# Performance work log

Hardware: AMD Instinct MI355X
Metric: run time of the kernel (lower is better)

## Reference

```python
import jax, jax.numpy as jnp
import numpy as np

EPSILON = 1e-5  # parameters.EPSILON
BN_EPS = 1e-5
N_NODES, N_EDGES, D = 50000, 400000, 128


def batch_norm(x, gamma, beta):
    # BatchNorm1d in training mode: biased batch statistics over dim 0
    m = jnp.mean(x, axis=0)
    v = jnp.var(x, axis=0)
    return (x - m) * jax.lax.rsqrt(v + BN_EPS) * gamma + beta


def setup_inputs() -> dict:
    key = jax.random.key(0)
    ks = jax.random.split(key, 16)
    s = 0.05
    d = D
    inp = {
        "h": jax.random.normal(ks[0], (N_NODES, d), jnp.float32),
        "e": jax.random.normal(ks[1], (N_EDGES, d), jnp.float32),
        "src": jax.random.randint(ks[2], (N_EDGES,), 0, N_NODES, jnp.int32),
        "dst": jax.random.randint(ks[3], (N_EDGES,), 0, N_NODES, jnp.int32),
        # weights stored [in, out]
        "W_emb_node": jax.random.normal(ks[4], (d, d)) * s,
        "W_emb_edge": jax.random.normal(ks[5], (d, d)) * s,
        "W_emb_eta": jax.random.normal(ks[6], (d, d)) * s,
        "Uw": jax.random.normal(ks[7], (d, d)) * s, "Ub": jnp.zeros((d,)),
        "Vw": jax.random.normal(ks[8], (d, d)) * s, "Vb": jnp.zeros((d,)),
        "W1w": jax.random.normal(ks[9], (d, d)) * s, "W1b": jnp.zeros((d,)),
        "W2w": jax.random.normal(ks[10], (d, d)) * s, "W2b": jnp.zeros((d,)),
        "W3w": jax.random.normal(ks[11], (d, d)) * s, "W3b": jnp.zeros((d,)),
        "h_gamma": jnp.ones((d,)), "h_beta": jnp.zeros((d,)),
        "e_gamma": jnp.ones((d,)), "e_beta": jnp.zeros((d,)),
    }
    return inp


def reference(h, e, src, dst, W_emb_node, W_emb_edge, W_emb_eta,
              Uw, Ub, Vw, Vb, W1w, W1b, W2w, W2b, W3w, W3b,
              h_gamma, h_beta, e_gamma, e_beta):
    n_nodes = h.shape[0]
    # node-level linear projections
    h_emb = h @ W_emb_node                 # [N, d]
    Uh = h @ Uw + Ub                       # [N, d]
    Vh = h @ Vw + Vb                       # [N, d]
    W2h = h @ W2w + W2b                    # [N, d]
    W3h = h @ W3w + W3b                    # [N, d]
    # edge-level
    e_emb = e @ W_emb_edge                 # [E, d]
    W1e = e @ W1w + W1b                    # [E, d]
    # edge update: e_ij = emb(e) + ReLU(BN(W1 e + W2 h_src + W3 h_dst))
    pre_e = W1e + W2h[src] + W3h[dst]      # gather [E, d]
    e_new = e_emb + jax.nn.relu(batch_norm(pre_e, e_gamma, e_beta))
    # gate: sigma_ij = embedding_eta(sigmoid(e_ij))
    sigma = jax.nn.sigmoid(e_new) @ W_emb_eta  # [E, d]
    # weighted-sum aggregation to destination nodes
    num = jax.ops.segment_sum(sigma * Vh[src], dst, num_segments=n_nodes)
    den = jax.ops.segment_sum(sigma, dst, num_segments=n_nodes)
    agg = num / (den + EPSILON)            # [N, d]
    h_new = h_emb + jax.nn.relu(batch_norm(Uh + agg, h_gamma, h_beta))
    return (h_new, e_new)
```

## Files before the change

### kernel.cpp

```cpp
#include <hip/hip_runtime.h>
#include <cstdint>
#include <cstddef>
#include <cmath>

#define DD 128

typedef short bf16x8 __attribute__((ext_vector_type(8)));
typedef float f32x4 __attribute__((ext_vector_type(4)));

static __device__ __forceinline__ short f2bf(float f){
  union { float f; uint32_t u; } v; v.f = f;
  uint32_t r = v.u + 0x7FFFu + ((v.u >> 16) & 1u);
  return (short)(r >> 16);
}
static __device__ __forceinline__ float bf2f(short h){
  union { uint32_t u; float f; } v; v.u = ((uint32_t)(uint16_t)h) << 16;
  return v.f;
}
static __device__ __forceinline__ double shfl_xor_f64(double v, int m){
  long long l = __double_as_longlong(v);
  int lo = (int)(l & 0xffffffffLL);
  int hi = (int)((unsigned long long)l >> 32);
  lo = __shfl_xor(lo, m, 64);
  hi = __shfl_xor(hi, m, 64);
  return __longlong_as_double(((long long)hi << 32) | (unsigned long long)(unsigned int)lo);
}

template<int EP>
__global__ __launch_bounds__(256, 2) void dgemm_k(
    const float* __restrict__ X,
    const float* __restrict__ W1, const float* __restrict__ b1,
    const float* __restrict__ W2, const float* __restrict__ b2,
    float* __restrict__ Y1, float* __restrict__ Y2,
    int M, int nTiles,
    const int* __restrict__ src, const int* __restrict__ dst,
    const float* __restrict__ T2, const float* __restrict__ T3,
    double* __restrict__ eSum, double* __restrict__ eSumSq)
{
  __shared__ float sA[128][36];
  __shared__ float sW1[32][128];
  __shared__ float sW2[32][128];
  __shared__ double redS[(EP == 1) ? 4 : 1][32][4];
  __shared__ double redQ[(EP == 1) ? 4 : 1][32][4];

  const int tid = threadIdx.x, tx = tid & 31, ty = tid >> 5;
  const int c0 = tx * 4, r0 = ty * 16;
  const int lane = tid & 63, wv = tid >> 6;

  float b1c[4], b2c[4];
  #pragma unroll
  for (int j = 0; j < 4; ++j){
    b1c[j] = b1 ? b1[c0 + j] : 0.0f;
    b2c[j] = b2 ? b2[c0 + j] : 0.0f;
  }
  double st_s[4] = {0,0,0,0}, st_q[4] = {0,0,0,0};

  #pragma unroll 1
  for (int tile = blockIdx.x; tile < nTiles; tile += gridDim.x){
    const int rowBase = tile * 128;
    float acc1[16][4], acc2[16][4];
    #pragma unroll
    for (int r = 0; r < 16; ++r)
      #pragma unroll
      for (int j = 0; j < 4; ++j){ acc1[r][j] = 0.0f; acc2[r][j] = 0.0f; }

    #pragma unroll 1
    for (int h = 0; h < 4; ++h){
      #pragma unroll
      for (int m = 0; m < 4; ++m){
        int k = ty + 8 * m;
        *(f32x4*)&sW1[k][c0] = *(const f32x4*)&W1[(size_t)(h*32 + k) * DD + c0];
        *(f32x4*)&sW2[k][c0] = *(const f32x4*)&W2[(size_t)(h*32 + k) * DD + c0];
      }
      {
        int r = tid >> 1, koff = (tid & 1) * 16;
        int ar = rowBase + r; if (ar >= M) ar = M - 1;
        const float* xp = X + (size_t)ar * DD + h*32 + koff;
        #pragma unroll
        for (int q = 0; q < 4; ++q)
          *(f32x4*)&sA[r][koff + q*4] = *(const f32x4*)(xp + q*4);
      }
      __syncthreads();

      #pragma unroll
      for (int q = 0; q < 8; ++q){
        f32x4 wA0 = *(const f32x4*)&sW1[4*q + 0][c0];
        f32x4 wA1 = *(const f32x4*)&sW1[4*q + 1][c0];
        f32x4 wA2 = *(const f32x4*)&sW1[4*q + 2][c0];
        f32x4 wA3 = *(const f32x4*)&sW1[4*q + 3][c0];
        f32x4 wB0 = *(const f32x4*)&sW2[4*q + 0][c0];
        f32x4 wB1 = *(const f32x4*)&sW2[4*q + 1][c0];
        f32x4 wB2 = *(const f32x4*)&sW2[4*q + 2][c0];
        f32x4 wB3 = *(const f32x4*)&sW2[4*q + 3][c0];
        #pragma unroll
        for (int r = 0; r < 16; ++r){
          f32x4 a = *(const f32x4*)&sA[r0 + r][4*q];
          #pragma unroll
          for (int j = 0; j < 4; ++j){
            float t1 = acc1[r][j];
            t1 = fmaf(a[0], wA0[j], t1); t1 = fmaf(a[1], wA1[j], t1);
            t1 = fmaf(a[2], wA2[j], t1); t1 = fmaf(a[3], wA3[j], t1);
            acc1[r][j] = t1;
            float t2 = acc2[r][j];
            t2 = fmaf(a[0], wB0[j], t2); t2 = fmaf(a[1], wB1[j], t2);
            t2 = fmaf(a[2], wB2[j], t2); t2 = fmaf(a[3], wB3[j], t2);
            acc2[r][j] = t2;
          }
        }
      }
      __syncthreads();
    }

    #pragma unroll
    for (int r = 0; r < 16; ++r){
      int row = rowBase + r0 + r;
      if (row < M){
        size_t base = (size_t)row * DD + c0;
        if (EP == 0){
          f32x4 o1, o2;
          #pragma unroll
          for (int j = 0; j < 4; ++j){ o1[j] = acc1[r][j] + b1c[j]; o2[j] = acc2[r][j] + b2c[j]; }
          *(f32x4*)&Y1[base] = o1;
          *(f32x4*)&Y2[base] = o2;
        } else {
          int s = src[row], d = dst[row];
          f32x4 t2v = *(const f32x4*)&T2[(size_t)s * DD + c0];
          f32x4 t3v = *(const f32x4*)&T3[(size_t)d * DD + c0];
          f32x4 o1, o2;
          #pragma unroll
          for (int j = 0; j < 4; ++j){
            o1[j] = ((acc1[r][j] + b1c[j]) + t2v[j]) + t3v[j];
            st_s[j] += (double)o1[j];
            st_q[j] += (double)o1[j] * (double)o1[j];
            o2[j] = acc2[r][j];
          }
          *(f32x4*)&Y1[base] = o1;
          *(f32x4*)&Y2[base] = o2;
        }
      }
    }
  }

  if (EP == 1){
    #pragma unroll
    for (int j = 0; j < 4; ++j){
      st_s[j] += shfl_xor_f64(st_s[j], 32);
      st_q[j] += shfl_xor_f64(st_q[j], 32);
    }
    if (lane < 32){
      #pragma unroll
      for (int j = 0; j < 4; ++j){ redS[wv][lane][j] = st_s[j]; redQ[wv][lane][j] = st_q[j]; }
    }
    __syncthreads();
    if (tid < 128){
      int txx = tid >> 2, j = tid & 3;
      double s = 0.0, q = 0.0;
      #pragma unroll
      for (int w = 0; w < 4; ++w){ s += redS[w][txx][j]; q += redQ[w][txx][j]; }
      atomicAdd(&eSum[txx*4 + j], s);
      atomicAdd(&eSumSq[txx*4 + j], q);
    }
  }
}

__global__ __launch_bounds__(256, 2) void sgemm_k(
    const float* __restrict__ preE, const float* __restrict__ eEmb,
    const float* __restrict__ Weta,
    float* __restrict__ eNew, float* __restrict__ sigmaOut,
    const float* __restrict__ mF, const float* __restrict__ rF,
    const float* __restrict__ gF, const float* __restrict__ bF,
    int M, int nTiles)
{
  __shared__ float sA[128][68];
  __shared__ float sW[64][128];
  const int tid = threadIdx.x, tx = tid & 31, ty = tid >> 5;
  const int c0 = tx * 4, r0 = ty * 16;

  #pragma unroll 1
  for (int tile = blockIdx.x; tile < nTiles; tile += gridDim.x){
    const int rowBase = tile * 128;
    float acc[16][4];
    #pragma unroll
    for (int r = 0; r < 16; ++r)
      #pragma unroll
      for (int j = 0; j < 4; ++j) acc[r][j] = 0.0f;

    #pragma unroll 1
    for (int h = 0; h < 2; ++h){
      {
        int kk = ty * 8;
        #pragma unroll
        for (int q = 0; q < 8; ++q)
          *(f32x4*)&sW[kk + q][c0] = *(const f32x4*)&Weta[(size_t)(h*64 + kk + q) * DD + c0];
      }
      {
        int r = tid >> 1, koff = (tid & 1) * 32;
        int ar = rowBase + r;
        int gcb = h*64 + koff;
        const float* pp = preE + (size_t)ar * DD + gcb;
        const float* ep = eEmb + (size_t)ar * DD + gcb;
        float* np = eNew + (size_t)ar * DD + gcb;
        #pragma unroll
        for (int q = 0; q < 8; ++q){
          f32x4 pe = *(const f32x4*)(pp + q*4);
          f32x4 em = *(const f32x4*)(ep + q*4);
          f32x4 mm = *(const f32x4*)&mF[gcb + q*4];
          f32x4 rr = *(const f32x4*)&rF[gcb + q*4];
          f32x4 gg = *(const f32x4*)&gF[gcb + q*4];
          f32x4 bb = *(const f32x4*)&bF[gcb + q*4];
          f32x4 en, sg;
          #pragma unroll
          for (int j = 0; j < 4; ++j){
            float xm  = pe[j] - mm[j];
            float t1  = xm * rr[j];
            float t2v = t1 * gg[j];
            float t3v = t2v + bb[j];
            float t = fmaxf(t3v, 0.0f);
            en[j] = em[j] + t;
            sg[j] = 1.0f / (1.0f + expf(-en[j]));
          }
          *(f32x4*)(np + q*4) = en;
          *(f32x4*)&sA[r][koff + q*4] = sg;
        }
      }
      __syncthreads();

      #pragma unroll 2
      for (int q = 0; q < 16; ++q){
        f32x4 b0 = *(const f32x4*)&sW[4*q + 0][c0];
        f32x4 b1 = *(const f32x4*)&sW[4*q + 1][c0];
        f32x4 b2 = *(const f32x4*)&sW[4*q + 2][c0];
        f32x4 b3 = *(const f32x4*)&sW[4*q + 3][c0];
        #pragma unroll
        for (int r = 0; r < 16; ++r){
          f32x4 a = *(const f32x4*)&sA[r0 + r][4*q];
          #pragma unroll
          for (int j = 0; j < 4; ++j){
            float t = acc[r][j];
            t = fmaf(a[0], b0[j], t); t = fmaf(a[1], b1[j], t);
            t = fmaf(a[2], b2[j], t); t = fmaf(a[3], b3[j], t);
            acc[r][j] = t;
          }
        }
      }
      __syncthreads();
    }

    #pragma unroll
    for (int r = 0; r < 16; ++r){
      int row = rowBase + r0 + r;
      f32x4 o;
      #pragma unroll
      for (int j = 0; j < 4; ++j) o[j] = acc[r][j];
      *(f32x4*)&sigmaOut[(size_t)row * DD + c0] = o;
    }
  }
}

__global__ void hist_k(const int* __restrict__ dst, int NE, int* __restrict__ counts){
  int i = blockIdx.x * blockDim.x + threadIdx.x;
  if (i < NE) atomicAdd(&counts[dst[i]], 1);
}

__global__ __launch_bounds__(1024, 1) void scan_k(const int* __restrict__ counts, int NN,
                                                  int* __restrict__ rowStart, int* __restrict__ cursor){
  __shared__ int part[1024];
  const int T = 1024, t = threadIdx.x;
  const int chunk = (NN + T - 1) / T;
  const int lo = t * chunk;
  const int hi = (lo + chunk < NN) ? lo + chunk : NN;
  int s = 0;
  for (int i = lo; i < hi; ++i) s += counts[i];
  part[t] = s;
  __syncthreads();
  for (int off = 1; off < T; off <<= 1){
    int v = (t >= off) ? part[t - off] : 0;
    __syncthreads();
    part[t] += v;
    __syncthreads();
  }
  int run = (t == 0) ? 0 : part[t - 1];
  for (int i = lo; i < hi; ++i){ rowStart[i] = run; cursor[i] = run; run += counts[i]; }
  if (t == T - 1) rowStart[NN] = run;
}

__global__ void place_k(const int* __restrict__ dst, int NE,
                        int* __restrict__ cursor, int* __restrict__ edgeIdx){
  int i = blockIdx.x * blockDim.x + threadIdx.x;
  if (i < NE){ int p = atomicAdd(&cursor[dst[i]], 1); edgeIdx[p] = i; }
}

__global__ __launch_bounds__(256, 4) void gather_k(
    const float* __restrict__ sigma, const float* __restrict__ Vh,
    const int* __restrict__ rowStart, const int* __restrict__ edgeIdx,
    const int* __restrict__ srcArr,
    const float* __restrict__ Uh, float* __restrict__ preH, int NN)
{
  const int lane = threadIdx.x & 63, wv = threadIdx.x >> 6;
  for (int node = blockIdx.x * 4 + wv; node < NN; node += gridDim.x * 4){
    const int beg = rowStart[node], end = rowStart[node + 1];
    float den0 = 0.f, den1 = 0.f, num0 = 0.f, num1 = 0.f;
    for (int eb = beg; eb < end; eb += 4){
      const int nE = end - eb;
      float sg0[4], sg1[4], vh0[4], vh1[4];
      #pragma unroll
      for (int q = 0; q < 4; ++q){
        if (q < nE){
          int eid = edgeIdx[eb + q];
          int s = srcArr[eid];
          sg0[q] = sigma[(size_t)eid * DD + lane];
          sg1[q] = sigma[(size_t)eid * DD + 64 + lane];
          vh0[q] = Vh[(size_t)s * DD + lane];
          vh1[q] = Vh[(size_t)s * DD + 64 + lane];
        } else { sg0[q] = 0.f; sg1[q] = 0.f; vh0[q] = 0.f; vh1[q] = 0.f; }
      }
      #pragma unroll
      for (int q = 0; q < 4; ++q){
        den0 += sg0[q]; den1 += sg1[q];
        num0 = fmaf(sg0[q], vh0[q], num0);
        num1 = fmaf(sg1[q], vh1[q], num1);
      }
    }
    const size_t b = (size_t)node * DD;
    preH[b + lane]      = Uh[b + lane]      + num0 / (den0 + 1e-5f);
    preH[b + 64 + lane] = Uh[b + 64 + lane] + num1 / (den1 + 1e-5f);
  }
}

__global__ void finalizeE_k(const double* __restrict__ sum, const double* __restrict__ sumsq,
                            double M, float* __restrict__ mF, float* __restrict__ rF)
{
  int c = threadIdx.x;
  double m = sum[c] / M;
  double v = sumsq[c] / M - m * m;
  float vf = (float)v;
  mF[c] = (float)m;
  rF[c] = 1.0f / sqrtf(vf + 1e-5f);
}

__global__ void stats64_k(const float* __restrict__ X, int M,
                          double* __restrict__ sum, double* __restrict__ sumsq)
{
  const int col = threadIdx.x & 127;
  const int half = threadIdx.x >> 7;
  double s = 0.0, q = 0.0;
  for (int r = blockIdx.x * 2 + half; r < M; r += gridDim.x * 2){
    double v = (double)X[(size_t)r * DD + col];
    s += v; q += v * v;
  }
  __shared__ double sS[256], sQ[256];
  sS[threadIdx.x] = s; sQ[threadIdx.x] = q;
  __syncthreads();
  if (half == 0){
    atomicAdd(&sum[col],   sS[col] + sS[col + 128]);
    atomicAdd(&sumsq[col], sQ[col] + sQ[col + 128]);
  }
}

__global__ void finalize64_k(const double* __restrict__ sum, const double* __restrict__ sumsq,
                             double M, const float* __restrict__ gamma, const float* __restrict__ beta,
                             double* __restrict__ scale, double* __restrict__ shift)
{
  int c = threadIdx.x;
  double m = sum[c] / M;
  double var = sumsq[c] / M - m * m;
  double sc = (double)gamma[c] / sqrt(var + 1e-5);
  scale[c] = sc;
  shift[c] = (double)beta[c] - m * sc;
}

__global__ __launch_bounds__(256, 2) void hfinal_mfma_k(
    const float* __restrict__ X, const float* __restrict__ W,
    float* __restrict__ Y, int M, int rowTiles,
    const float* __restrict__ preH,
    const double* __restrict__ hSc, const double* __restrict__ hSh)
{
  const int tid = threadIdx.x;
  const int lane = tid & 63;
  const int wv = tid >> 6;
  const int l15 = lane & 15;
  const int lg = lane >> 4;
  const int colBase = blockIdx.y * 64;

  __shared__ short sW[2][64][136];
  for (int t = tid; t < 64 * 128; t += 256){
    int k = t >> 6, nl = t & 63;
    float w = W[k * DD + colBase + nl];
    short hi = f2bf(w);
    sW[0][nl][k] = hi;
    sW[1][nl][k] = f2bf(w - bf2f(hi));
  }
  __syncthreads();

  bf16x8 Bhi[4][4], Blo[4][4];
  #pragma unroll
  for (int ct = 0; ct < 4; ++ct)
    #pragma unroll
    for (int ks = 0; ks < 4; ++ks){
      Bhi[ct][ks] = *(const bf16x8*)&sW[0][ct*16 + l15][ks*32 + lg*8];
      Blo[ct][ks] = *(const bf16x8*)&sW[1][ct*16 + l15][ks*32 + lg*8];
    }

  for (int rt = blockIdx.x; rt < rowTiles; rt += gridDim.x){
    int arow = rt * 64 + wv * 16 + l15;
    if (arow >= M) arow = M - 1;
    const f32x4* xr = (const f32x4*)(X + (size_t)arow * DD);

    bf16x8 Ahi[4], Alo[4];
    #pragma unroll
    for (int ks = 0; ks < 4; ++ks){
      f32x4 a0 = xr[ks*8 + lg*2];
      f32x4 a1 = xr[ks*8 + lg*2 + 1];
      float av[8];
      #pragma unroll
      for (int j = 0; j < 4; ++j){ av[j] = a0[j]; av[4+j] = a1[j]; }
      #pragma unroll
      for (int j = 0; j < 8; ++j){
        short hi = f2bf(av[j]);
        Ahi[ks][j] = hi;
        Alo[ks][j] = f2bf(av[j] - bf2f(hi));
      }
    }

    f32x4 acc[4];
    #pragma unroll
    for (int ct = 0; ct < 4; ++ct) acc[ct] = (f32x4){0.f, 0.f, 0.f, 0.f};
    #pragma unroll
    for (int ct = 0; ct < 4; ++ct)
      #pragma unroll
      for (int ks = 0; ks < 4; ++ks){
        acc[ct] = __builtin_amdgcn_mfma_f32_16x16x32_bf16(Ahi[ks], Bhi[ct][ks], acc[ct], 0, 0, 0);
        acc[ct] = __builtin_amdgcn_mfma_f32_16x16x32_bf16(Ahi[ks], Blo[ct][ks], acc[ct], 0, 0, 0);
        acc[ct] = __builtin_amdgcn_mfma_f32_16x16x32_bf16(Alo[ks], Bhi[ct][ks], acc[ct], 0, 0, 0);
      }

    const int r0 = rt * 64 + wv * 16 + lg * 4;
    #pragma unroll
    for (int reg = 0; reg < 4; ++reg){
      int r = r0 + reg;
      if (r < M){
        #pragma unroll
        for (int ct = 0; ct < 4; ++ct){
          int c = colBase + ct*16 + l15;
          double t = (double)preH[(size_t)r * DD + c] * hSc[c] + hSh[c];
          float tv = t > 0.0 ? (float)t : 0.0f;
          Y[(size_t)r * DD + c] = acc[ct][reg] + tv;
        }
      }
    }
  }
}

extern "C" void kernel_launch(void* const* d_in, const int* in_sizes, int n_in,
                              void* d_out, int out_size, void* d_ws, size_t ws_size,
                              hipStream_t stream)
{
  const float* h  = (const float*)d_in[0];
  const float* e  = (const float*)d_in[1];
  const int* src  = (const int*)d_in[2];
  const int* dst  = (const int*)d_in[3];
  const float* Wemb_n   = (const float*)d_in[4];
  const float* Wemb_e   = (const float*)d_in[5];
  const float* Wemb_eta = (const float*)d_in[6];
  const float* Uw  = (const float*)d_in[7];  const float* Ub  = (const float*)d_in[8];
  const float* Vw  = (const float*)d_in[9];  const float* Vb  = (const float*)d_in[10];
  const float* W1w = (const float*)d_in[11]; const float* W1b = (const float*)d_in[12];
  const float* W2w = (const float*)d_in[13]; const float* W2b = (const float*)d_in[14];
  const float* W3w = (const float*)d_in[15]; const float* W3b = (const float*)d_in[16];
  const float* h_gamma = (const float*)d_in[17]; const float* h_beta = (const float*)d_in[18];
  const float* e_gamma = (const float*)d_in[19]; const float* e_beta = (const float*)d_in[20];

  const int NN = in_sizes[0] / DD;
  const int NE = in_sizes[2];

  char* wsp = (char*)d_ws;
  float* W2h    = (float*)wsp;  wsp += (size_t)NN * DD * sizeof(float);
  float* W3h    = (float*)wsp;  wsp += (size_t)NN * DD * sizeof(float);
  float* Vh     = (float*)wsp;  wsp += (size_t)NN * DD * sizeof(float);
  float* embSig = (float*)wsp;  wsp += (size_t)NE * DD * sizeof(float);
  double* stats = (double*)wsp; wsp += 6 * DD * sizeof(double);
  double* eSum = stats;        double* eSumSq = stats + DD;
  double* hSum = stats + 2*DD; double* hSumSq = stats + 3*DD;
  double* hScale = stats + 4*DD; double* hShift = stats + 5*DD;
  float* mF = (float*)wsp;   wsp += DD * sizeof(float);
  float* rF = (float*)wsp;   wsp += DD * sizeof(float);
  int* counts   = (int*)wsp; wsp += (size_t)NN * sizeof(int);
  int* rowStart = (int*)wsp; wsp += ((size_t)NN + 1) * sizeof(int);
  int* cursor   = (int*)wsp; wsp += (size_t)NN * sizeof(int);
  int* edgeIdx  = (int*)wsp; wsp += (size_t)NE * sizeof(int);

  float* h_new_out = (float*)d_out;
  float* e_out     = (float*)d_out + (size_t)NN * DD;

  const int tN = (NN + 127) / 128;
  const int tE = (NE + 127) / 128;
  const int rtN64 = (NN + 63) / 64;
  dim3 blk(256);

  hipMemsetAsync(stats, 0, (size_t)4 * DD * sizeof(double), stream);
  hipMemsetAsync(counts, 0, (size_t)NN * sizeof(int), stream);

  hist_k<<<(NE + 255) / 256, blk, 0, stream>>>(dst, NE, counts);
  scan_k<<<1, 1024, 0, stream>>>(counts, NN, rowStart, cursor);
  place_k<<<(NE + 255) / 256, blk, 0, stream>>>(dst, NE, cursor, edgeIdx);

  dgemm_k<0><<<tN, blk, 0, stream>>>(h, Uw, Ub, Vw, Vb, h_new_out, Vh, NN, tN,
      nullptr, nullptr, nullptr, nullptr, nullptr, nullptr);
  dgemm_k<0><<<tN, blk, 0, stream>>>(h, W2w, W2b, W3w, W3b, W2h, W3h, NN, tN,
      nullptr, nullptr, nullptr, nullptr, nullptr, nullptr);

  dgemm_k<1><<<1024, blk, 0, stream>>>(e, W1w, W1b, Wemb_e, nullptr, e_out, embSig,
      NE, tE, src, dst, W2h, W3h, eSum, eSumSq);

  finalizeE_k<<<1, 128, 0, stream>>>(eSum, eSumSq, (double)NE, mF, rF);

  sgemm_k<<<tE, blk, 0, stream>>>(e_out, embSig, Wemb_eta, e_out, embSig,
      mF, rF, e_gamma, e_beta, NE, tE);

  gather_k<<<(NN + 3) / 4, blk, 0, stream>>>(embSig, Vh, rowStart, edgeIdx, src,
      h_new_out, h_new_out, NN);

  stats64_k<<<512, blk, 0, stream>>>(h_new_out, NN, hSum, hSumSq);
  finalize64_k<<<1, 128, 0, stream>>>(hSum, hSumSq, (double)NN, h_gamma, h_beta, hScale, hShift);

  hfinal_mfma_k<<<dim3(rtN64, 2), blk, 0, stream>>>(h, Wemb_n, h_new_out, NN, rtN64,
      h_new_out, hScale, hShift);
}
```

Baseline: 1.251 ms.

## Use 512-thread blocks with halved per-thread tiles, merge node GEMM launches

Thread blocks for the FP32 GEMM kernels go from 256 to 512 threads, and each thread now holds 8 rows instead of 16. This halves accumulator registers and lets more waves fit per CU to hide latency. The two node-level dgemm launches are merged into one grid, using blockIdx.y to pick the weight set, and sgemm now uses a persistent grid of 1024 blocks with smaller K chunks. The gather loop is widened to 8 edges per iteration for more memory-level parallelism. Costs are more shared-memory loads per FMA, since the register tile is smaller, and more barriers.

```diff
diff --git a/kernel.cpp b/kernel.cpp
--- a/kernel.cpp
+++ b/kernel.cpp
@@ -27,11 +27,14 @@
 }
 
 template<int EP>
-__global__ __launch_bounds__(256, 2) void dgemm_k(
+__global__ __launch_bounds__(512, 4) void dgemm_k(
     const float* __restrict__ X,
-    const float* __restrict__ W1, const float* __restrict__ b1,
-    const float* __restrict__ W2, const float* __restrict__ b2,
-    float* __restrict__ Y1, float* __restrict__ Y2,
+    const float* __restrict__ W1a, const float* __restrict__ b1a,
+    const float* __restrict__ W2a, const float* __restrict__ b2a,
+    float* __restrict__ Y1a, float* __restrict__ Y2a,
+    const float* __restrict__ W1B, const float* __restrict__ b1B,
+    const float* __restrict__ W2B, const float* __restrict__ b2B,
+    float* __restrict__ Y1B, float* __restrict__ Y2B,
     int M, int nTiles,
     const int* __restrict__ src, const int* __restrict__ dst,
     const float* __restrict__ T2, const float* __restrict__ T3,
@@ -40,12 +43,18 @@
   __shared__ float sA[128][36];
   __shared__ float sW1[32][128];
   __shared__ float sW2[32][128];
-  __shared__ double redS[(EP == 1) ? 4 : 1][32][4];
-  __shared__ double redQ[(EP == 1) ? 4 : 1][32][4];
+  __shared__ double redS[(EP == 1) ? 8 : 1][32][4];
+  __shared__ double redQ[(EP == 1) ? 8 : 1][32][4];
 
   const int tid = threadIdx.x, tx = tid & 31, ty = tid >> 5;
-  const int c0 = tx * 4, r0 = ty * 16;
+  const int c0 = tx * 4, r0 = ty * 8;
   const int lane = tid & 63, wv = tid >> 6;
+
+  const float *W1 = W1a, *b1 = b1a, *W2 = W2a, *b2 = b2a;
+  float *Y1 = Y1a, *Y2 = Y2a;
+  if (EP == 0 && blockIdx.y == 1){
+    W1 = W1B; b1 = b1B; W2 = W2B; b2 = b2B; Y1 = Y1B; Y2 = Y2B;
+  }
 
   float b1c[4], b2c[4];
   #pragma unroll
@@ -58,27 +67,27 @@
   #pragma unroll 1
   for (int tile = blockIdx.x; tile < nTiles; tile += gridDim.x){
     const int rowBase = tile * 128;
-    float acc1[16][4], acc2[16][4];
-    #pragma unroll
-    for (int r = 0; r < 16; ++r)
+    float acc1[8][4], acc2[8][4];
+    #pragma unroll
+    for (int r = 0; r < 8; ++r)
       #pragma unroll
       for (int j = 0; j < 4; ++j){ acc1[r][j] = 0.0f; acc2[r][j] = 0.0f; }
 
     #pragma unroll 1
     for (int h = 0; h < 4; ++h){
       #pragma unroll
-      for (int m = 0; m < 4; ++m){
-        int k = ty + 8 * m;
-        *(f32x4*)&sW1[k][c0] = *(const f32x4*)&W1[(size_t)(h*32 + k) * DD + c0];
-        *(f32x4*)&sW2[k][c0] = *(const f32x4*)&W2[(size_t)(h*32 + k) * DD + c0];
+      for (int m = 0; m < 2; ++m){
+        int idx = tid + m * 512;
+        int k = idx >> 5, cc = (idx & 31) * 4;
+        *(f32x4*)&sW1[k][cc] = *(const f32x4*)&W1[(size_t)(h*32 + k) * DD + cc];
+        *(f32x4*)&sW2[k][cc] = *(const f32x4*)&W2[(size_t)(h*32 + k) * DD + cc];
       }
       {
-        int r = tid >> 1, koff = (tid & 1) * 16;
+        int r = tid >> 2, koff = (tid & 3) * 8;
         int ar = rowBase + r; if (ar >= M) ar = M - 1;
         const float* xp = X + (size_t)ar * DD + h*32 + koff;
-        #pragma unroll
-        for (int q = 0; q < 4; ++q)
-          *(f32x4*)&sA[r][koff + q*4] = *(const f32x4*)(xp + q*4);
+        *(f32x4*)&sA[r][koff]     = *(const f32x4*)(xp);
+        *(f32x4*)&sA[r][koff + 4] = *(const f32x4*)(xp + 4);
       }
       __syncthreads();
 
@@ -93,7 +102,7 @@
         f32x4 wB2 = *(const f32x4*)&sW2[4*q + 2][c0];
         f32x4 wB3 = *(const f32x4*)&sW2[4*q + 3][c0];
         #pragma unroll
-        for (int r = 0; r < 16; ++r){
+        for (int r = 0; r < 8; ++r){
           f32x4 a = *(const f32x4*)&sA[r0 + r][4*q];
           #pragma unroll
           for (int j = 0; j < 4; ++j){
@@ -112,7 +121,7 @@
     }
 
     #pragma unroll
-    for (int r = 0; r < 16; ++r){
+    for (int r = 0; r < 8; ++r){
       int row = rowBase + r0 + r;
       if (row < M){
         size_t base = (size_t)row * DD + c0;
@@ -156,14 +165,14 @@
       int txx = tid >> 2, j = tid & 3;
       double s = 0.0, q = 0.0;
       #pragma unroll
-      for (int w = 0; w < 4; ++w){ s += redS[w][txx][j]; q += redQ[w][txx][j]; }
+      for (int w = 0; w < 8; ++w){ s += redS[w][txx][j]; q += redQ[w][txx][j]; }
       atomicAdd(&eSum[txx*4 + j], s);
       atomicAdd(&eSumSq[txx*4 + j], q);
     }
   }
 }
 
-__global__ __launch_bounds__(256, 2) void sgemm_k(
+__global__ __launch_bounds__(512, 4) void sgemm_k(
     const float* __restrict__ preE, const float* __restrict__ eEmb,
     const float* __restrict__ Weta,
     float* __restrict__ eNew, float* __restrict__ sigmaOut,
@@ -171,37 +180,37 @@
     const float* __restrict__ gF, const float* __restrict__ bF,
     int M, int nTiles)
 {
-  __shared__ float sA[128][68];
-  __shared__ float sW[64][128];
+  __shared__ float sA[128][36];
+  __shared__ float sW[32][128];
   const int tid = threadIdx.x, tx = tid & 31, ty = tid >> 5;
-  const int c0 = tx * 4, r0 = ty * 16;
+  const int c0 = tx * 4, r0 = ty * 8;
 
   #pragma unroll 1
   for (int tile = blockIdx.x; tile < nTiles; tile += gridDim.x){
     const int rowBase = tile * 128;
-    float acc[16][4];
-    #pragma unroll
-    for (int r = 0; r < 16; ++r)
+    float acc[8][4];
+    #pragma unroll
+    for (int r = 0; r < 8; ++r)
       #pragma unroll
       for (int j = 0; j < 4; ++j) acc[r][j] = 0.0f;
 
     #pragma unroll 1
-    for (int h = 0; h < 2; ++h){
+    for (int h = 0; h < 4; ++h){
+      #pragma unroll
+      for (int m = 0; m < 2; ++m){
+        int idx = tid + m * 512;
+        int k = idx >> 5, cc = (idx & 31) * 4;
+        *(f32x4*)&sW[k][cc] = *(const f32x4*)&Weta[(size_t)(h*32 + k) * DD + cc];
+      }
       {
-        int kk = ty * 8;
-        #pragma unroll
-        for (int q = 0; q < 8; ++q)
-          *(f32x4*)&sW[kk + q][c0] = *(const f32x4*)&Weta[(size_t)(h*64 + kk + q) * DD + c0];
-      }
-      {
-        int r = tid >> 1, koff = (tid & 1) * 32;
+        int r = tid >> 2, koff = (tid & 3) * 8;
         int ar = rowBase + r;
-        int gcb = h*64 + koff;
+        int gcb = h*32 + koff;
         const float* pp = preE + (size_t)ar * DD + gcb;
         const float* ep = eEmb + (size_t)ar * DD + gcb;
         float* np = eNew + (size_t)ar * DD + gcb;
         #pragma unroll
-        for (int q = 0; q < 8; ++q){
+        for (int q = 0; q < 2; ++q){
           f32x4 pe = *(const f32x4*)(pp + q*4);
           f32x4 em = *(const f32x4*)(ep + q*4);
           f32x4 mm = *(const f32x4*)&mF[gcb + q*4];
@@ -225,14 +234,14 @@
       }
       __syncthreads();
 
-      #pragma unroll 2
-      for (int q = 0; q < 16; ++q){
+      #pragma unroll
+      for (int q = 0; q < 8; ++q){
         f32x4 b0 = *(const f32x4*)&sW[4*q + 0][c0];
         f32x4 b1 = *(const f32x4*)&sW[4*q + 1][c0];
         f32x4 b2 = *(const f32x4*)&sW[4*q + 2][c0];
         f32x4 b3 = *(const f32x4*)&sW[4*q + 3][c0];
         #pragma unroll
-        for (int r = 0; r < 16; ++r){
+        for (int r = 0; r < 8; ++r){
           f32x4 a = *(const f32x4*)&sA[r0 + r][4*q];
           #pragma unroll
           for (int j = 0; j < 4; ++j){
@@ -247,7 +256,7 @@
     }
 
     #pragma unroll
-    for (int r = 0; r < 16; ++r){
+    for (int r = 0; r < 8; ++r){
       int row = rowBase + r0 + r;
       f32x4 o;
       #pragma unroll
@@ -300,11 +309,11 @@
   for (int node = blockIdx.x * 4 + wv; node < NN; node += gridDim.x * 4){
     const int beg = rowStart[node], end = rowStart[node + 1];
     float den0 = 0.f, den1 = 0.f, num0 = 0.f, num1 = 0.f;
-    for (int eb = beg; eb < end; eb += 4){
+    for (int eb = beg; eb < end; eb += 8){
       const int nE = end - eb;
-      float sg0[4], sg1[4], vh0[4], vh1[4];
-      #pragma unroll
-      for (int q = 0; q < 4; ++q){
+      float sg0[8], sg1[8], vh0[8], vh1[8];
+      #pragma unroll
+      for (int q = 0; q < 8; ++q){
         if (q < nE){
           int eid = edgeIdx[eb + q];
           int s = srcArr[eid];
@@ -315,7 +324,7 @@
         } else { sg0[q] = 0.f; sg1[q] = 0.f; vh0[q] = 0.f; vh1[q] = 0.f; }
       }
       #pragma unroll
-      for (int q = 0; q < 4; ++q){
+      for (int q = 0; q < 8; ++q){
         den0 += sg0[q]; den1 += sg1[q];
         num0 = fmaf(sg0[q], vh0[q], num0);
         num1 = fmaf(sg1[q], vh1[q], num1);
@@ -495,34 +504,36 @@
   const int tN = (NN + 127) / 128;
   const int tE = (NE + 127) / 128;
   const int rtN64 = (NN + 63) / 64;
-  dim3 blk(256);
+  dim3 blk256(256), blk512(512);
 
   hipMemsetAsync(stats, 0, (size_t)4 * DD * sizeof(double), stream);
   hipMemsetAsync(counts, 0, (size_t)NN * sizeof(int), stream);
 
-  hist_k<<<(NE + 255) / 256, blk, 0, stream>>>(dst, NE, counts);
+  hist_k<<<(NE + 255) / 256, blk256, 0, stream>>>(dst, NE, counts);
   scan_k<<<1, 1024, 0, stream>>>(counts, NN, rowStart, cursor);
-  place_k<<<(NE + 255) / 256, blk, 0, stream>>>(dst, NE, cursor, edgeIdx);
-
-  dgemm_k<0><<<tN, blk, 0, stream>>>(h, Uw, Ub, Vw, Vb, h_new_out, Vh, NN, tN,
-      nullptr, nullptr, nullptr, nullptr, nullptr, nullptr);
-  dgemm_k<0><<<tN, blk, 0, stream>>>(h, W2w, W2b, W3w, W3b, W2h, W3h, NN, tN,
-      nullptr, nullptr, nullptr, nullptr, nullptr, nullptr);
-
-  dgemm_k<1><<<1024, blk, 0, stream>>>(e, W1w, W1b, Wemb_e, nullptr, e_out, embSig,
+  place_k<<<(NE + 255) / 256, blk256, 0, stream>>>(dst, NE, cursor, edgeIdx);
+
+  dgemm_k<0><<<dim3(256, 2), blk512, 0, stream>>>(h,
+      Uw, Ub, Vw, Vb, h_new_out, Vh,
+      W2w, W2b, W3w, W3b, W2h, W3h,
+      NN, tN, nullptr, nullptr, nullptr, nullptr, nullptr, nullptr);
+
+  dgemm_k<1><<<1024, blk512, 0, stream>>>(e,
+      W1w, W1b, Wemb_e, nullptr, e_out, embSig,
+      nullptr, nullptr, nullptr, nullptr, nullptr, nullptr,
       NE, tE, src, dst, W2h, W3h, eSum, eSumSq);
 
   finalizeE_k<<<1, 128, 0, stream>>>(eSum, eSumSq, (double)NE, mF, rF);
 
-  sgemm_k<<<tE, blk, 0, stream>>>(e_out, embSig, Wemb_eta, e_out, embSig,
+  sgemm_k<<<1024, blk512, 0, stream>>>(e_out, embSig, Wemb_eta, e_out, embSig,
       mF, rF, e_gamma, e_beta, NE, tE);
 
-  gather_k<<<(NN + 3) / 4, blk, 0, stream>>>(embSig, Vh, rowStart, edgeIdx, src,
+  gather_k<<<(NN + 3) / 4, blk256, 0, stream>>>(embSig, Vh, rowStart, edgeIdx, src,
       h_new_out, h_new_out, NN);
 
-  stats64_k<<<512, blk, 0, stream>>>(h_new_out, NN, hSum, hSumSq);
+  stats64_k<<<512, blk256, 0, stream>>>(h_new_out, NN, hSum, hSumSq);
   finalize64_k<<<1, 128, 0, stream>>>(hSum, hSumSq, (double)NN, h_gamma, h_beta, hScale, hShift);
 
-  hfinal_mfma_k<<<dim3(rtN64, 2), blk, 0, stream>>>(h, Wemb_n, h_new_out, NN, rtN64,
+  hfinal_mfma_k<<<dim3(rtN64, 2), blk256, 0, stream>>>(h, Wemb_n, h_new_out, NN, rtN64,
       h_new_out, hScale, hShift);
 }
```

Result: slower. 1.370 ms (+9.6%).

## Split dual-output GEMMs into single-output GEMMs and shrink sigmoid-GEMM tiles

Applied to the files above, without the earlier changes.

Replaces the dual-weight GEMM kernel with a single-weight version, so each node projection and the edge embedding run as separate launches with half the accumulators and shared memory. The sigmoid/eta GEMM now uses 32-wide K chunks, caches BN parameters in shared memory, and runs on a persistent 1024-block grid. The gather loop processes 8 edges per iteration instead of 4. Register pressure and LDS use go down, which can raise occupancy, but X (h and e) is read twice as often, and the edge tensor e is now read twice.

```diff
diff --git a/kernel.cpp b/kernel.cpp
--- a/kernel.cpp
+++ b/kernel.cpp
@@ -27,84 +27,72 @@
 }
 
 template<int EP>
-__global__ __launch_bounds__(256, 2) void dgemm_k(
-    const float* __restrict__ X,
-    const float* __restrict__ W1, const float* __restrict__ b1,
-    const float* __restrict__ W2, const float* __restrict__ b2,
-    float* __restrict__ Y1, float* __restrict__ Y2,
+__global__ __launch_bounds__(256, 2) void fgemm_k(
+    const float* __restrict__ X, const float* __restrict__ W,
+    const float* __restrict__ bias, float* __restrict__ Y,
     int M, int nTiles,
     const int* __restrict__ src, const int* __restrict__ dst,
     const float* __restrict__ T2, const float* __restrict__ T3,
     double* __restrict__ eSum, double* __restrict__ eSumSq)
 {
   __shared__ float sA[128][36];
-  __shared__ float sW1[32][128];
-  __shared__ float sW2[32][128];
+  __shared__ float sW[32][128];
   __shared__ double redS[(EP == 1) ? 4 : 1][32][4];
   __shared__ double redQ[(EP == 1) ? 4 : 1][32][4];
 
   const int tid = threadIdx.x, tx = tid & 31, ty = tid >> 5;
   const int c0 = tx * 4, r0 = ty * 16;
   const int lane = tid & 63, wv = tid >> 6;
-
-  float b1c[4], b2c[4];
+  const int sa_r = tid >> 1, sa_k = (tid & 1) * 16;
+  const int sw_k = tid >> 3, sw_c = (tid & 7) * 16;
+
+  float bias_c[4];
   #pragma unroll
-  for (int j = 0; j < 4; ++j){
-    b1c[j] = b1 ? b1[c0 + j] : 0.0f;
-    b2c[j] = b2 ? b2[c0 + j] : 0.0f;
-  }
+  for (int j = 0; j < 4; ++j) bias_c[j] = bias ? bias[c0 + j] : 0.0f;
+
   double st_s[4] = {0,0,0,0}, st_q[4] = {0,0,0,0};
 
   #pragma unroll 1
   for (int tile = blockIdx.x; tile < nTiles; tile += gridDim.x){
     const int rowBase = tile * 128;
-    float acc1[16][4], acc2[16][4];
+    float acc[16][4];
     #pragma unroll
     for (int r = 0; r < 16; ++r)
       #pragma unroll
-      for (int j = 0; j < 4; ++j){ acc1[r][j] = 0.0f; acc2[r][j] = 0.0f; }
+      for (int j = 0; j < 4; ++j) acc[r][j] = 0.0f;
 
     #pragma unroll 1
     for (int h = 0; h < 4; ++h){
-      #pragma unroll
-      for (int m = 0; m < 4; ++m){
-        int k = ty + 8 * m;
-        *(f32x4*)&sW1[k][c0] = *(const f32x4*)&W1[(size_t)(h*32 + k) * DD + c0];
-        *(f32x4*)&sW2[k][c0] = *(const f32x4*)&W2[(size_t)(h*32 + k) * DD + c0];
-      }
       {
-        int r = tid >> 1, koff = (tid & 1) * 16;
-        int ar = rowBase + r; if (ar >= M) ar = M - 1;
-        const float* xp = X + (size_t)ar * DD + h*32 + koff;
-        #pragma unroll
-        for (int q = 0; q < 4; ++q)
-          *(f32x4*)&sA[r][koff + q*4] = *(const f32x4*)(xp + q*4);
+        const float* wp = W + (size_t)(h*32 + sw_k) * DD + sw_c;
+        #pragma unroll
+        for (int i = 0; i < 4; ++i)
+          *(f32x4*)&sW[sw_k][sw_c + i*4] = *(const f32x4*)(wp + i*4);
+      }
+      {
+        int ar = rowBase + sa_r; if (ar >= M) ar = M - 1;
+        const float* xp = X + (size_t)ar * DD + h*32 + sa_k;
+        #pragma unroll
+        for (int i = 0; i < 4; ++i)
+          *(f32x4*)&sA[sa_r][sa_k + i*4] = *(const f32x4*)(xp + i*4);
       }
       __syncthreads();
 
       #pragma unroll
       for (int q = 0; q < 8; ++q){
-        f32x4 wA0 = *(const f32x4*)&sW1[4*q + 0][c0];
-        f32x4 wA1 = *(const f32x4*)&sW1[4*q + 1][c0];
-        f32x4 wA2 = *(const f32x4*)&sW1[4*q + 2][c0];
-        f32x4 wA3 = *(const f32x4*)&sW1[4*q + 3][c0];
-        f32x4 wB0 = *(const f32x4*)&sW2[4*q + 0][c0];
-        f32x4 wB1 = *(const f32x4*)&sW2[4*q + 1][c0];
-        f32x4 wB2 = *(const f32x4*)&sW2[4*q + 2][c0];
-        f32x4 wB3 = *(const f32x4*)&sW2[4*q + 3][c0];
+        f32x4 b0 = *(const f32x4*)&sW[4*q + 0][c0];
+        f32x4 b1 = *(const f32x4*)&sW[4*q + 1][c0];
+        f32x4 b2 = *(const f32x4*)&sW[4*q + 2][c0];
+        f32x4 b3 = *(const f32x4*)&sW[4*q + 3][c0];
         #pragma unroll
         for (int r = 0; r < 16; ++r){
           f32x4 a = *(const f32x4*)&sA[r0 + r][4*q];
           #pragma unroll
           for (int j = 0; j < 4; ++j){
-            float t1 = acc1[r][j];
-            t1 = fmaf(a[0], wA0[j], t1); t1 = fmaf(a[1], wA1[j], t1);
-            t1 = fmaf(a[2], wA2[j], t1); t1 = fmaf(a[3], wA3[j], t1);
-            acc1[r][j] = t1;
-            float t2 = acc2[r][j];
-            t2 = fmaf(a[0], wB0[j], t2); t2 = fmaf(a[1], wB1[j], t2);
-            t2 = fmaf(a[2], wB2[j], t2); t2 = fmaf(a[3], wB3[j], t2);
-            acc2[r][j] = t2;
+            float t = acc[r][j];
+            t = fmaf(a[0], b0[j], t); t = fmaf(a[1], b1[j], t);
+            t = fmaf(a[2], b2[j], t); t = fmaf(a[3], b3[j], t);
+            acc[r][j] = t;
           }
         }
       }
@@ -117,25 +105,22 @@
       if (row < M){
         size_t base = (size_t)row * DD + c0;
         if (EP == 0){
-          f32x4 o1, o2;
+          f32x4 o;
           #pragma unroll
-          for (int j = 0; j < 4; ++j){ o1[j] = acc1[r][j] + b1c[j]; o2[j] = acc2[r][j] + b2c[j]; }
-          *(f32x4*)&Y1[base] = o1;
-          *(f32x4*)&Y2[base] = o2;
+          for (int j = 0; j < 4; ++j) o[j] = acc[r][j] + bias_c[j];
+          *(f32x4*)&Y[base] = o;
         } else {
           int s = src[row], d = dst[row];
-          f32x4 t2v = *(const f32x4*)&T2[(size_t)s * DD + c0];
-          f32x4 t3v = *(const f32x4*)&T3[(size_t)d * DD + c0];
-          f32x4 o1, o2;
+          f32x4 t2 = *(const f32x4*)&T2[(size_t)s * DD + c0];
+          f32x4 t3 = *(const f32x4*)&T3[(size_t)d * DD + c0];
+          f32x4 o;
           #pragma unroll
           for (int j = 0; j < 4; ++j){
-            o1[j] = ((acc1[r][j] + b1c[j]) + t2v[j]) + t3v[j];
-            st_s[j] += (double)o1[j];
-            st_q[j] += (double)o1[j] * (double)o1[j];
-            o2[j] = acc2[r][j];
+            o[j] = ((acc[r][j] + bias_c[j]) + t2[j]) + t3[j];
+            st_s[j] += (double)o[j];
+            st_q[j] += (double)o[j] * (double)o[j];
           }
-          *(f32x4*)&Y1[base] = o1;
-          *(f32x4*)&Y2[base] = o2;
+          *(f32x4*)&Y[base] = o;
         }
       }
     }
@@ -163,7 +148,7 @@
   }
 }
 
-__global__ __launch_bounds__(256, 2) void sgemm_k(
+__global__ __launch_bounds__(256, 2) void psgemm_k(
     const float* __restrict__ preE, const float* __restrict__ eEmb,
     const float* __restrict__ Weta,
     float* __restrict__ eNew, float* __restrict__ sigmaOut,
@@ -171,14 +156,26 @@
     const float* __restrict__ gF, const float* __restrict__ bF,
     int M, int nTiles)
 {
-  __shared__ float sA[128][68];
-  __shared__ float sW[64][128];
+  __shared__ float sA[128][36];
+  __shared__ float sW[32][128];
+  __shared__ float sBN[4][128];
+
   const int tid = threadIdx.x, tx = tid & 31, ty = tid >> 5;
   const int c0 = tx * 4, r0 = ty * 16;
+  const int sa_r = tid >> 1, sa_k = (tid & 1) * 16;
+  const int sw_k = tid >> 3, sw_c = (tid & 7) * 16;
+
+  if (tid < 128){
+    sBN[0][tid] = mF[tid]; sBN[1][tid] = rF[tid];
+    sBN[2][tid] = gF[tid]; sBN[3][tid] = bF[tid];
+  }
+  __syncthreads();
 
   #pragma unroll 1
   for (int tile = blockIdx.x; tile < nTiles; tile += gridDim.x){
     const int rowBase = tile * 128;
+    const int ar = rowBase + sa_r;
+
     float acc[16][4];
     #pragma unroll
     for (int r = 0; r < 16; ++r)
@@ -186,28 +183,26 @@
       for (int j = 0; j < 4; ++j) acc[r][j] = 0.0f;
 
     #pragma unroll 1
-    for (int h = 0; h < 2; ++h){
+    for (int h = 0; h < 4; ++h){
       {
-        int kk = ty * 8;
-        #pragma unroll
-        for (int q = 0; q < 8; ++q)
-          *(f32x4*)&sW[kk + q][c0] = *(const f32x4*)&Weta[(size_t)(h*64 + kk + q) * DD + c0];
+        const float* wp = Weta + (size_t)(h*32 + sw_k) * DD + sw_c;
+        #pragma unroll
+        for (int i = 0; i < 4; ++i)
+          *(f32x4*)&sW[sw_k][sw_c + i*4] = *(const f32x4*)(wp + i*4);
       }
       {
-        int r = tid >> 1, koff = (tid & 1) * 32;
-        int ar = rowBase + r;
-        int gcb = h*64 + koff;
+        int gcb = h*32 + sa_k;
         const float* pp = preE + (size_t)ar * DD + gcb;
         const float* ep = eEmb + (size_t)ar * DD + gcb;
         float* np = eNew + (size_t)ar * DD + gcb;
         #pragma unroll
-        for (int q = 0; q < 8; ++q){
-          f32x4 pe = *(const f32x4*)(pp + q*4);
-          f32x4 em = *(const f32x4*)(ep + q*4);
-          f32x4 mm = *(const f32x4*)&mF[gcb + q*4];
-          f32x4 rr = *(const f32x4*)&rF[gcb + q*4];
-          f32x4 gg = *(const f32x4*)&gF[gcb + q*4];
-          f32x4 bb = *(const f32x4*)&bF[gcb + q*4];
+        for (int i = 0; i < 4; ++i){
+          f32x4 pe = *(const f32x4*)(pp + i*4);
+          f32x4 em = *(const f32x4*)(ep + i*4);
+          f32x4 mm = *(const f32x4*)&sBN[0][gcb + i*4];
+          f32x4 rr = *(const f32x4*)&sBN[1][gcb + i*4];
+          f32x4 gg = *(const f32x4*)&sBN[2][gcb + i*4];
+          f32x4 bb = *(const f32x4*)&sBN[3][gcb + i*4];
           f32x4 en, sg;
           #pragma unroll
           for (int j = 0; j < 4; ++j){
@@ -219,14 +214,14 @@
             en[j] = em[j] + t;
             sg[j] = 1.0f / (1.0f + expf(-en[j]));
           }
-          *(f32x4*)(np + q*4) = en;
-          *(f32x4*)&sA[r][koff + q*4] = sg;
+          *(f32x4*)(np + i*4) = en;
+          *(f32x4*)&sA[sa_r][sa_k + i*4] = sg;
         }
       }
       __syncthreads();
 
-      #pragma unroll 2
-      for (int q = 0; q < 16; ++q){
+      #pragma unroll
+      for (int q = 0; q < 8; ++q){
         f32x4 b0 = *(const f32x4*)&sW[4*q + 0][c0];
         f32x4 b1 = *(const f32x4*)&sW[4*q + 1][c0];
         f32x4 b2 = *(const f32x4*)&sW[4*q + 2][c0];
@@ -300,11 +295,11 @@
   for (int node = blockIdx.x * 4 + wv; node < NN; node += gridDim.x * 4){
     const int beg = rowStart[node], end = rowStart[node + 1];
     float den0 = 0.f, den1 = 0.f, num0 = 0.f, num1 = 0.f;
-    for (int eb = beg; eb < end; eb += 4){
+    for (int eb = beg; eb < end; eb += 8){
       const int nE = end - eb;
-      float sg0[4], sg1[4], vh0[4], vh1[4];
-      #pragma unroll
-      for (int q = 0; q < 4; ++q){
+      float sg0[8], sg1[8], vh0[8], vh1[8];
+      #pragma unroll
+      for (int q = 0; q < 8; ++q){
         if (q < nE){
           int eid = edgeIdx[eb + q];
           int s = srcArr[eid];
@@ -315,7 +310,7 @@
         } else { sg0[q] = 0.f; sg1[q] = 0.f; vh0[q] = 0.f; vh1[q] = 0.f; }
       }
       #pragma unroll
-      for (int q = 0; q < 4; ++q){
+      for (int q = 0; q < 8; ++q){
         den0 += sg0[q]; den1 += sg1[q];
         num0 = fmaf(sg0[q], vh0[q], num0);
         num1 = fmaf(sg1[q], vh1[q], num1);
@@ -495,34 +490,41 @@
   const int tN = (NN + 127) / 128;
   const int tE = (NE + 127) / 128;
   const int rtN64 = (NN + 63) / 64;
-  dim3 blk(256);
+  dim3 blk256(256);
 
   hipMemsetAsync(stats, 0, (size_t)4 * DD * sizeof(double), stream);
   hipMemsetAsync(counts, 0, (size_t)NN * sizeof(int), stream);
 
-  hist_k<<<(NE + 255) / 256, blk, 0, stream>>>(dst, NE, counts);
+  hist_k<<<(NE + 255) / 256, blk256, 0, stream>>>(dst, NE, counts);
   scan_k<<<1, 1024, 0, stream>>>(counts, NN, rowStart, cursor);
-  place_k<<<(NE + 255) / 256, blk, 0, stream>>>(dst, NE, cursor, edgeIdx);
-
-  dgemm_k<0><<<tN, blk, 0, stream>>>(h, Uw, Ub, Vw, Vb, h_new_out, Vh, NN, tN,
+  place_k<<<(NE + 255) / 256, blk256, 0, stream>>>(dst, NE, cursor, edgeIdx);
+
+  fgemm_k<0><<<tN, blk256, 0, stream>>>(h, Uw, Ub, h_new_out, NN, tN,
       nullptr, nullptr, nullptr, nullptr, nullptr, nullptr);
-  dgemm_k<0><<<tN, blk, 0, stream>>>(h, W2w, W2b, W3w, W3b, W2h, W3h, NN, tN,
+  fgemm_k<0><<<tN, blk256, 0, stream>>>(h, Vw, Vb, Vh, NN, tN,
       nullptr, nullptr, nullptr, nullptr, nullptr, nullptr);
-
-  dgemm_k<1><<<1024, blk, 0, stream>>>(e, W1w, W1b, Wemb_e, nullptr, e_out, embSig,
-      NE, tE, src, dst, W2h, W3h, eSum, eSumSq);
+  fgemm_k<0><<<tN, blk256, 0, stream>>>(h, W2w, W2b, W2h, NN, tN,
+      nullptr, nullptr, nullptr, nullptr, nullptr, nullptr);
+  fgemm_k<0><<<tN, blk256, 0, stream>>>(h, W3w, W3b, W3h, NN, tN,
+      nullptr, nullptr, nullptr, nullptr, nullptr, nullptr);
+
+  fgemm_k<1><<<1024, blk256, 0, stream>>>(e, W1w, W1b, e_out, NE, tE,
+      src, dst, W2h, W3h, eSum, eSumSq);
 
   finalizeE_k<<<1, 128, 0, stream>>>(eSum, eSumSq, (double)NE, mF, rF);
 
-  sgemm_k<<<tE, blk, 0, stream>>>(e_out, embSig, Wemb_eta, e_out, embSig,
+  fgemm_k<0><<<1024, blk256, 0, stream>>>(e, Wemb_e, nullptr, embSig, NE, tE,
+      nullptr, nullptr, nullptr, nullptr, nullptr, nullptr);
+
+  psgemm_k<<<1024, blk256, 0, stream>>>(e_out, embSig, Wemb_eta, e_out, embSig,
       mF, rF, e_gamma, e_beta, NE, tE);
 
-  gather_k<<<(NN + 3) / 4, blk, 0, stream>>>(embSig, Vh, rowStart, edgeIdx, src,
+  gather_k<<<(NN + 3) / 4, blk256, 0, stream>>>(embSig, Vh, rowStart, edgeIdx, src,
       h_new_out, h_new_out, NN);
 
-  stats64_k<<<512, blk, 0, stream>>>(h_new_out, NN, hSum, hSumSq);
+  stats64_k<<<512, blk256, 0, stream>>>(h_new_out, NN, hSum, hSumSq);
   finalize64_k<<<1, 128, 0, stream>>>(hSum, hSumSq, (double)NN, h_gamma, h_beta, hScale, hShift);
 
-  hfinal_mfma_k<<<dim3(rtN64, 2), blk, 0, stream>>>(h, Wemb_n, h_new_out, NN, rtN64,
+  hfinal_mfma_k<<<dim3(rtN64, 2), blk256, 0, stream>>>(h, Wemb_n, h_new_out, NN, rtN64,
       h_new_out, hScale, hShift);
 }
```

After: 1.127 ms. 1.11x faster.
